# Performance work log

Hardware: AMD Instinct MI355X
Metric: run time of the kernel (lower is better)

## Reference

```python
import jax, jax.numpy as jnp
import numpy as np

NEG = -1e6  # masked_softmax fill value from the original code


def setup_inputs() -> dict:
    key = jax.random.key(0)
    ks = jax.random.split(key, 8)
    B, Q, K, Dq, Dk, Dv, H = 8, 256, 1024, 256, 256, 128, 128
    queries = jax.random.normal(ks[0], (B, Q, Dq), dtype=jnp.float32)
    keys = jax.random.normal(ks[1], (B, K, Dk), dtype=jnp.float32)
    values = jax.random.normal(ks[2], (B, K, Dv), dtype=jnp.float32)
    valid_lens = jax.random.randint(ks[3], (B,), 1, K + 1, dtype=jnp.int32)
    # learned params (Dense, use_bias=False): y = x @ W
    W_q = jax.random.normal(ks[4], (Dq, H), dtype=jnp.float32) / np.sqrt(Dq)
    W_k = jax.random.normal(ks[5], (Dk, H), dtype=jnp.float32) / np.sqrt(Dk)
    w_v = jax.random.normal(ks[6], (H,), dtype=jnp.float32) / np.sqrt(H)
    return {"queries": queries, "keys": keys, "values": values,
            "valid_lens": valid_lens, "W_q": W_q, "W_k": W_k, "w_v": w_v}


def reference(queries, keys, values, valid_lens, W_q, W_k, w_v):
    q = jnp.einsum('bqd,dh->bqh', queries, W_q)          # [B,Q,H]
    k = jnp.einsum('bkd,dh->bkh', keys, W_k)             # [B,K,H]
    features = jnp.tanh(q[:, :, None, :] + k[:, None, :, :])  # [B,Q,K,H]
    scores = jnp.einsum('bqkh,h->bqk', features, w_v)    # [B,Q,K]
    # masked softmax over last axis: positions >= valid_len set to -1e6
    K_len = scores.shape[-1]
    mask = jnp.arange(K_len)[None, None, :] < valid_lens[:, None, None]
    scores = jnp.where(mask, scores, NEG)
    attn = jax.nn.softmax(scores, axis=-1)
    return jnp.einsum('bqk,bkv->bqv', attn, values)      # [B,Q,Dv]
```

## Files before the change

kernel.cpp:

```cpp
#include <hip/hip_runtime.h>
#include <hip/hip_bf16.h>

#if defined(__has_builtin)
#if __has_builtin(__builtin_amdgcn_exp2f)
#define EXP2F __builtin_amdgcn_exp2f
#endif
#if __has_builtin(__builtin_amdgcn_rcpf)
#define RCPF __builtin_amdgcn_rcpf
#endif
#endif
#ifndef EXP2F
#define EXP2F exp2f
#endif
#ifndef RCPF
#define RCPF(x) (1.0f / (x))
#endif

#define B_  8
#define Q_  256
#define K_  1024
#define D_  256
#define H_  128
#define DV_ 128

#define CSL 2.8853900817779268f
#define L2E 1.4426950408889634f

#define QE_OFF   0
#define KE_OFF   262144
#define WPK_OFF  1310720
#define PART_OFF 1311744
#define PSZ      1310720

__global__ __launch_bounds__(256) void proj_split(
    const float* __restrict__ queries, const float* __restrict__ keys,
    const float* __restrict__ Wq, const float* __restrict__ Wk,
    float* __restrict__ part, int nchunk)
{
    __shared__ __align__(16) float As[64][68];
    __shared__ __align__(16) float Ws[64][128];

    const int tid = threadIdx.x;
    const int rt = blockIdx.x;
    const bool isQ = rt < 32;
    const int row0 = isQ ? rt * 64 : (rt - 32) * 64;
    const int crow0 = isQ ? row0 : row0 + 2048;
    const float* A = isQ ? (queries + row0 * D_) : (keys + row0 * D_);
    const float* W = isQ ? Wq : Wk;

    float acc[8][4];
#pragma unroll
    for (int i = 0; i < 8; i++)
#pragma unroll
        for (int j = 0; j < 4; j++) acc[i][j] = 0.f;

    const int rgrp = tid >> 5;
    const int c0 = (tid & 31) * 4;
    const int lr = tid & 63;
    const int ld = (tid >> 6) * 16;

    for (int ch = 0; ch < nchunk; ch++) {
        const int d0 = (blockIdx.y * nchunk + ch) * 64;
#pragma unroll
        for (int j = 0; j < 4; j++) {
            const float4 a = *(const float4*)&A[lr * D_ + d0 + ld + j * 4];
            As[ld + j * 4 + 0][lr] = a.x;
            As[ld + j * 4 + 1][lr] = a.y;
            As[ld + j * 4 + 2][lr] = a.z;
            As[ld + j * 4 + 3][lr] = a.w;
        }
#pragma unroll
        for (int l = 0; l < 8; l++) {
            const int idx = tid + l * 256;
            const int rr = idx >> 5, cc = (idx & 31) * 4;
            *(float4*)&Ws[rr][cc] = *(const float4*)&W[(d0 + rr) * H_ + cc];
        }
        __syncthreads();
#pragma unroll 4
        for (int d = 0; d < 64; d++) {
            const float4 w = *(const float4*)&Ws[d][c0];
            const float4 a0 = *(const float4*)&As[d][rgrp * 8];
            const float4 a1 = *(const float4*)&As[d][rgrp * 8 + 4];
            const float ar[8] = {a0.x, a0.y, a0.z, a0.w, a1.x, a1.y, a1.z, a1.w};
#pragma unroll
            for (int i = 0; i < 8; i++) {
                acc[i][0] = fmaf(ar[i], w.x, acc[i][0]);
                acc[i][1] = fmaf(ar[i], w.y, acc[i][1]);
                acc[i][2] = fmaf(ar[i], w.z, acc[i][2]);
                acc[i][3] = fmaf(ar[i], w.w, acc[i][3]);
            }
        }
        __syncthreads();
    }
    float* dst = part + (size_t)blockIdx.y * PSZ + (size_t)(crow0 + rgrp * 8) * H_ + c0;
#pragma unroll
    for (int i = 0; i < 8; i++)
        *(float4*)&dst[i * H_] = make_float4(acc[i][0], acc[i][1], acc[i][2], acc[i][3]);
}

__global__ __launch_bounds__(256) void finish_kernel(
    const float* __restrict__ part, int S,
    const float* __restrict__ w_v,
    float* __restrict__ qE, float* __restrict__ kET, float* __restrict__ wpk)
{
    __shared__ float T[128][33];
    const int tid = threadIdx.x;
    const int row0 = blockIdx.x * 32;
    const bool isQ = row0 < 2048;

    float e[16];
#pragma unroll
    for (int i = 0; i < 16; i++) {
        const int idx = row0 * H_ + tid + i * 256;
        float v = part[idx];
        for (int s = 1; s < S; s++) v += part[(size_t)s * PSZ + idx];
        e[i] = EXP2F(CSL * v);
    }
    if (isQ) {
#pragma unroll
        for (int i = 0; i < 16; i++) qE[row0 * H_ + tid + i * 256] = e[i];
    } else {
#pragma unroll
        for (int i = 0; i < 16; i++) {
            const int idx = tid + i * 256;
            T[idx & 127][idx >> 7] = e[i];
        }
        __syncthreads();
        const int krow0 = row0 - 2048;
        const int b = krow0 >> 10, k0 = krow0 & 1023;
        const int h = tid >> 1, kh = (tid & 1) * 16;
        float* dst = kET + (size_t)b * (H_ * K_) + (size_t)h * K_ + k0 + kh;
#pragma unroll
        for (int j = 0; j < 4; j++)
            *(float4*)&dst[j * 4] = make_float4(T[h][kh + j * 4], T[h][kh + j * 4 + 1],
                                                T[h][kh + j * 4 + 2], T[h][kh + j * 4 + 3]);
    }
    if (blockIdx.x == 0 && tid < 64) {
        const float w1 = -2.0f * L2E * w_v[2 * tid];
        const float w2 = -2.0f * L2E * w_v[2 * tid + 1];
        *(float4*)&wpk[tid * 4] = make_float4(w1, w2, w1 + w2, 0.f);
    }
}

__global__ void wpk_kernel(const float* __restrict__ w_v, float* __restrict__ wpk) {
    const int t = threadIdx.x;
    const float w1 = -2.0f * L2E * w_v[2 * t];
    const float w2 = -2.0f * L2E * w_v[2 * t + 1];
    *(float4*)&wpk[t * 4] = make_float4(w1, w2, w1 + w2, 0.f);
}

__global__ __launch_bounds__(256) void proj_direct(
    const float* __restrict__ queries, const float* __restrict__ keys,
    const float* __restrict__ Wq, const float* __restrict__ Wk,
    float* __restrict__ qE, float* __restrict__ kE)
{
    __shared__ __align__(16) float As[16][36];
    __shared__ __align__(16) float Ws[32][128];

    const int tid = threadIdx.x;
    const int blk = blockIdx.x;
    const bool isQ = blk < 128;
    const int row0 = isQ ? blk * 16 : (blk - 128) * 16;
    const float* A = isQ ? (queries + row0 * D_) : (keys + row0 * D_);
    const float* W = isQ ? Wq : Wk;

    float acc[8];
#pragma unroll
    for (int j = 0; j < 8; j++) acc[j] = 0.f;
    const int r = tid >> 4;
    const int c8 = (tid & 15) * 8;

    for (int d0 = 0; d0 < D_; d0 += 32) {
        if (tid < 128) {
            const int rr = tid >> 3, cc = (tid & 7) * 4;
            *(float4*)&As[rr][cc] = *(const float4*)&A[rr * D_ + d0 + cc];
        }
#pragma unroll
        for (int l = 0; l < 4; l++) {
            const int idx = tid + l * 256;
            const int rr = idx >> 5, cc = (idx & 31) * 4;
            *(float4*)&Ws[rr][cc] = *(const float4*)&W[(d0 + rr) * H_ + cc];
        }
        __syncthreads();
#pragma unroll
        for (int d = 0; d < 32; d++) {
            const float a = As[r][d];
            const float4 w0 = *(const float4*)&Ws[d][c8];
            const float4 w1 = *(const float4*)&Ws[d][c8 + 4];
            acc[0] = fmaf(a, w0.x, acc[0]); acc[1] = fmaf(a, w0.y, acc[1]);
            acc[2] = fmaf(a, w0.z, acc[2]); acc[3] = fmaf(a, w0.w, acc[3]);
            acc[4] = fmaf(a, w1.x, acc[4]); acc[5] = fmaf(a, w1.y, acc[5]);
            acc[6] = fmaf(a, w1.z, acc[6]); acc[7] = fmaf(a, w1.w, acc[7]);
        }
        __syncthreads();
    }
    float e[8];
#pragma unroll
    for (int j = 0; j < 8; j++) e[j] = EXP2F(CSL * acc[j]);
    if (isQ) {
        float* dst = qE + (row0 + r) * H_ + c8;
        *(float4*)dst = make_float4(e[0], e[1], e[2], e[3]);
        *(float4*)(dst + 4) = make_float4(e[4], e[5], e[6], e[7]);
    } else {
        const int krow = row0 + r;
        const int b = krow >> 10, k = krow & 1023;
        float* dst = kE + b * (H_ * K_) + c8 * K_ + k;
#pragma unroll
        for (int j = 0; j < 8; j++) dst[j * K_] = e[j];
    }
}

__global__ __launch_bounds__(1024, 8) void attn_kernel(
    const float* __restrict__ qE,
    const float* __restrict__ kET,
    const float* __restrict__ values,
    const int*   __restrict__ valid_lens,
    const float* __restrict__ wpk,
    float* __restrict__ out)
{
    __shared__ __align__(16) float sc[K_][4];
    __shared__ __align__(16) float red[16][4][128];
    __shared__ __align__(16) float psum[16][4];
    __shared__ float rl[4];

    const int tid = threadIdx.x;
    const int b  = blockIdx.y;
    const int q0 = blockIdx.x * 4;

    const float* q0p = qE + (b * Q_ + q0) * H_;
    const float* q1p = q0p + H_;
    const float* q2p = q0p + 2 * H_;
    const float* q3p = q0p + 3 * H_;
    const float* kb = kET + (size_t)b * (H_ * K_) + tid;

    float2 acc01 = make_float2(0.f, 0.f);
    float2 acc23 = make_float2(0.f, 0.f);

#pragma unroll 4
    for (int p = 0; p < 64; p++) {
        const float ek1 = kb[(2 * p) * K_];
        const float ek2 = kb[(2 * p + 1) * K_];
        const float4 wp = *(const float4*)&wpk[p * 4];
        const float2 qa = *(const float2*)&q0p[2 * p];
        const float2 qb = *(const float2*)&q1p[2 * p];
        const float2 qc = *(const float2*)&q2p[2 * p];
        const float2 qd = *(const float2*)&q3p[2 * p];
        {
            float2 x1 = make_float2(qa.x * ek1, qb.x * ek1);
            float2 x2 = make_float2(qa.y * ek2, qb.y * ek2);
            float2 e1 = make_float2(x1.x + 1.f, x1.y + 1.f);
            float2 d  = make_float2(fmaf(e1.x, x2.x, e1.x), fmaf(e1.y, x2.y, e1.y));
            float2 n  = make_float2(fmaf(wp.y, x1.x, wp.z), fmaf(wp.y, x1.y, wp.z));
            n = make_float2(fmaf(wp.x, x2.x, n.x), fmaf(wp.x, x2.y, n.y));
            acc01.x = fmaf(n.x, RCPF(d.x), acc01.x);
            acc01.y = fmaf(n.y, RCPF(d.y), acc01.y);
        }
        {
            float2 x1 = make_float2(qc.x * ek1, qd.x * ek1);
            float2 x2 = make_float2(qc.y * ek2, qd.y * ek2);
            float2 e1 = make_float2(x1.x + 1.f, x1.y + 1.f);
            float2 d  = make_float2(fmaf(e1.x, x2.x, e1.x), fmaf(e1.y, x2.y, e1.y));
            float2 n  = make_float2(fmaf(wp.y, x1.x, wp.z), fmaf(wp.y, x1.y, wp.z));
            n = make_float2(fmaf(wp.x, x2.x, n.x), fmaf(wp.x, x2.y, n.y));
            acc23.x = fmaf(n.x, RCPF(d.x), acc23.x);
            acc23.y = fmaf(n.y, RCPF(d.y), acc23.y);
        }
    }

    const int vl = valid_lens[b];
    const bool valid = tid < vl;
    float4 pv;
    pv.x = valid ? EXP2F(acc01.x) : 0.f;
    pv.y = valid ? EXP2F(acc01.y) : 0.f;
    pv.z = valid ? EXP2F(acc23.x) : 0.f;
    pv.w = valid ? EXP2F(acc23.y) : 0.f;
    *(float4*)&sc[tid][0] = pv;

    float4 s = pv;
#pragma unroll
    for (int sh = 32; sh > 0; sh >>= 1) {
        s.x += __shfl_xor(s.x, sh);
        s.y += __shfl_xor(s.y, sh);
        s.z += __shfl_xor(s.z, sh);
        s.w += __shfl_xor(s.w, sh);
    }
    const int lane = tid & 63, w = tid >> 6;
    if (lane == 0) *(float4*)&psum[w][0] = s;
    __syncthreads();
    if (tid < 4) {
        float t = 0.f;
#pragma unroll
        for (int ww = 0; ww < 16; ww++) t += psum[ww][tid];
        rl[tid] = RCPF(t);
    }

    const int vg = (tid & 31) * 4;
    const int kh = (tid >> 5) & 1;
    const int kc = tid >> 6;
    const float* vb = values + (size_t)b * (K_ * DV_) + vg;
    float av[4][4];
#pragma unroll
    for (int q = 0; q < 4; q++)
#pragma unroll
        for (int j = 0; j < 4; j++) av[q][j] = 0.f;
#pragma unroll 2
    for (int i = 0; i < 32; i++) {
        const int k = kc * 64 + i * 2 + kh;
        const float4 vv = *(const float4*)&vb[k * DV_];
        const float4 p = *(const float4*)&sc[k][0];
        av[0][0] = fmaf(p.x, vv.x, av[0][0]); av[0][1] = fmaf(p.x, vv.y, av[0][1]);
        av[0][2] = fmaf(p.x, vv.z, av[0][2]); av[0][3] = fmaf(p.x, vv.w, av[0][3]);
        av[1][0] = fmaf(p.y, vv.x, av[1][0]); av[1][1] = fmaf(p.y, vv.y, av[1][1]);
        av[1][2] = fmaf(p.y, vv.z, av[1][2]); av[1][3] = fmaf(p.y, vv.w, av[1][3]);
        av[2][0] = fmaf(p.z, vv.x, av[2][0]); av[2][1] = fmaf(p.z, vv.y, av[2][1]);
        av[2][2] = fmaf(p.z, vv.z, av[2][2]); av[2][3] = fmaf(p.z, vv.w, av[2][3]);
        av[3][0] = fmaf(p.w, vv.x, av[3][0]); av[3][1] = fmaf(p.w, vv.y, av[3][1]);
        av[3][2] = fmaf(p.w, vv.z, av[3][2]); av[3][3] = fmaf(p.w, vv.w, av[3][3]);
    }
#pragma unroll
    for (int q = 0; q < 4; q++)
#pragma unroll
        for (int j = 0; j < 4; j++) av[q][j] += __shfl_xor(av[q][j], 32);
    if (kh == 0) {
#pragma unroll
        for (int q = 0; q < 4; q++)
            *(float4*)&red[kc][q][vg] = make_float4(av[q][0], av[q][1], av[q][2], av[q][3]);
    }
    __syncthreads();

    if (tid < 512) {
        const int q = tid >> 7, v = tid & 127;
        float t = 0.f;
#pragma unroll
        for (int g = 0; g < 16; g++) t += red[g][q][v];
        out[(b * Q_ + q0 + q) * DV_ + v] = t * rl[q];
    }
}

extern "C" void kernel_launch(void* const* d_in, const int* in_sizes, int n_in,
                              void* d_out, int out_size, void* d_ws, size_t ws_size,
                              hipStream_t stream) {
    const float* queries    = (const float*)d_in[0];
    const float* keys       = (const float*)d_in[1];
    const float* values     = (const float*)d_in[2];
    const int*   valid_lens = (const int*)d_in[3];
    const float* W_q        = (const float*)d_in[4];
    const float* W_k        = (const float*)d_in[5];
    const float* w_v        = (const float*)d_in[6];
    float* out = (float*)d_out;

    float* ws  = (float*)d_ws;
    float* qE  = ws + QE_OFF;
    float* kET = ws + KE_OFF;
    float* wpk = ws + WPK_OFF;
    float* part = ws + PART_OFF;

    int S = 0;
    if (ws_size >= (size_t)(PART_OFF + 4 * (size_t)PSZ) * 4) S = 4;
    else if (ws_size >= (size_t)(PART_OFF + 2 * (size_t)PSZ) * 4) S = 2;
    else if (ws_size >= (size_t)(PART_OFF + 1 * (size_t)PSZ) * 4) S = 1;

    if (S > 0) {
        proj_split<<<dim3(160, S), 256, 0, stream>>>(queries, keys, W_q, W_k, part, 4 / S);
        finish_kernel<<<320, 256, 0, stream>>>(part, S, w_v, qE, kET, wpk);
    } else {
        proj_direct<<<640, 256, 0, stream>>>(queries, keys, W_q, W_k, qE, kET);
        wpk_kernel<<<1, 64, 0, stream>>>(w_v, wpk);
    }
    attn_kernel<<<dim3(Q_ / 4, B_), 1024, 0, stream>>>(qE, kET, values, valid_lens, wpk, out);
}
```

Before: 140.1 us.

## Fuse projection into one kernel, pack keys as float2, skip masked keys

Replaces the split-K projection and its separate finish kernel with a single projection kernel. That kernel applies the exponent and writes qE plus an h-pair-interleaved float2 key layout directly, which removes one launch and the partial-sum round trip. The attention kernel reads both key features of a pair with one float2 load, skips the score computation for keys beyond valid_len, and limits the P·V loop to valid keys. The single-kernel projection uses only 160 blocks with the full D reduction each, so it has less parallelism than the split version. Skipping work depends on the data-dependent valid lengths and causes divergence at the boundary.

```diff
diff --git a/kernel.cpp b/kernel.cpp
--- a/kernel.cpp
+++ b/kernel.cpp
@@ -29,45 +29,42 @@
 #define QE_OFF   0
 #define KE_OFF   262144
 #define WPK_OFF  1310720
-#define PART_OFF 1311744
-#define PSZ      1310720
-
-__global__ __launch_bounds__(256) void proj_split(
+
+__global__ __launch_bounds__(256) void proj_kernel(
     const float* __restrict__ queries, const float* __restrict__ keys,
     const float* __restrict__ Wq, const float* __restrict__ Wk,
-    float* __restrict__ part, int nchunk)
+    const float* __restrict__ w_v,
+    float* __restrict__ qE, float2* __restrict__ kET2, float* __restrict__ wpk)
 {
     __shared__ __align__(16) float As[64][68];
     __shared__ __align__(16) float Ws[64][128];
 
     const int tid = threadIdx.x;
-    const int rt = blockIdx.x;
-    const bool isQ = rt < 32;
-    const int row0 = isQ ? rt * 64 : (rt - 32) * 64;
-    const int crow0 = isQ ? row0 : row0 + 2048;
+    const int blk = blockIdx.x;
+    const bool isQ = blk < 32;
+    const int row0 = isQ ? blk * 64 : (blk - 32) * 64;
     const float* A = isQ ? (queries + row0 * D_) : (keys + row0 * D_);
     const float* W = isQ ? Wq : Wk;
 
-    float acc[8][4];
-#pragma unroll
-    for (int i = 0; i < 8; i++)
-#pragma unroll
-        for (int j = 0; j < 4; j++) acc[i][j] = 0.f;
-
-    const int rgrp = tid >> 5;
-    const int c0 = (tid & 31) * 4;
-    const int lr = tid & 63;
-    const int ld = (tid >> 6) * 16;
-
-    for (int ch = 0; ch < nchunk; ch++) {
-        const int d0 = (blockIdx.y * nchunk + ch) * 64;
+    float acc[4][8];
+#pragma unroll
+    for (int i = 0; i < 4; i++)
+#pragma unroll
+        for (int j = 0; j < 8; j++) acc[i][j] = 0.f;
+
+    const int lr  = tid & 63;
+    const int ldb = (tid >> 6) * 16;
+    const int r4  = (tid >> 4) * 4;
+    const int c8  = (tid & 15) * 8;
+
+    for (int d0 = 0; d0 < D_; d0 += 64) {
 #pragma unroll
         for (int j = 0; j < 4; j++) {
-            const float4 a = *(const float4*)&A[lr * D_ + d0 + ld + j * 4];
-            As[ld + j * 4 + 0][lr] = a.x;
-            As[ld + j * 4 + 1][lr] = a.y;
-            As[ld + j * 4 + 2][lr] = a.z;
-            As[ld + j * 4 + 3][lr] = a.w;
+            const float4 a = *(const float4*)&A[lr * D_ + d0 + ldb + j * 4];
+            As[ldb + j * 4 + 0][lr] = a.x;
+            As[ldb + j * 4 + 1][lr] = a.y;
+            As[ldb + j * 4 + 2][lr] = a.z;
+            As[ldb + j * 4 + 3][lr] = a.w;
         }
 #pragma unroll
         for (int l = 0; l < 8; l++) {
@@ -78,141 +75,54 @@
         __syncthreads();
 #pragma unroll 4
         for (int d = 0; d < 64; d++) {
-            const float4 w = *(const float4*)&Ws[d][c0];
-            const float4 a0 = *(const float4*)&As[d][rgrp * 8];
-            const float4 a1 = *(const float4*)&As[d][rgrp * 8 + 4];
-            const float ar[8] = {a0.x, a0.y, a0.z, a0.w, a1.x, a1.y, a1.z, a1.w};
-#pragma unroll
-            for (int i = 0; i < 8; i++) {
-                acc[i][0] = fmaf(ar[i], w.x, acc[i][0]);
-                acc[i][1] = fmaf(ar[i], w.y, acc[i][1]);
-                acc[i][2] = fmaf(ar[i], w.z, acc[i][2]);
-                acc[i][3] = fmaf(ar[i], w.w, acc[i][3]);
+            const float4 a4 = *(const float4*)&As[d][r4];
+            const float4 w0 = *(const float4*)&Ws[d][c8];
+            const float4 w1 = *(const float4*)&Ws[d][c8 + 4];
+            const float ar[4] = {a4.x, a4.y, a4.z, a4.w};
+#pragma unroll
+            for (int i = 0; i < 4; i++) {
+                acc[i][0] = fmaf(ar[i], w0.x, acc[i][0]);
+                acc[i][1] = fmaf(ar[i], w0.y, acc[i][1]);
+                acc[i][2] = fmaf(ar[i], w0.z, acc[i][2]);
+                acc[i][3] = fmaf(ar[i], w0.w, acc[i][3]);
+                acc[i][4] = fmaf(ar[i], w1.x, acc[i][4]);
+                acc[i][5] = fmaf(ar[i], w1.y, acc[i][5]);
+                acc[i][6] = fmaf(ar[i], w1.z, acc[i][6]);
+                acc[i][7] = fmaf(ar[i], w1.w, acc[i][7]);
             }
         }
         __syncthreads();
     }
-    float* dst = part + (size_t)blockIdx.y * PSZ + (size_t)(crow0 + rgrp * 8) * H_ + c0;
-#pragma unroll
-    for (int i = 0; i < 8; i++)
-        *(float4*)&dst[i * H_] = make_float4(acc[i][0], acc[i][1], acc[i][2], acc[i][3]);
-}
-
-__global__ __launch_bounds__(256) void finish_kernel(
-    const float* __restrict__ part, int S,
-    const float* __restrict__ w_v,
-    float* __restrict__ qE, float* __restrict__ kET, float* __restrict__ wpk)
-{
-    __shared__ float T[128][33];
-    const int tid = threadIdx.x;
-    const int row0 = blockIdx.x * 32;
-    const bool isQ = row0 < 2048;
-
-    float e[16];
-#pragma unroll
-    for (int i = 0; i < 16; i++) {
-        const int idx = row0 * H_ + tid + i * 256;
-        float v = part[idx];
-        for (int s = 1; s < S; s++) v += part[(size_t)s * PSZ + idx];
-        e[i] = EXP2F(CSL * v);
-    }
-    if (isQ) {
-#pragma unroll
-        for (int i = 0; i < 16; i++) qE[row0 * H_ + tid + i * 256] = e[i];
-    } else {
-#pragma unroll
-        for (int i = 0; i < 16; i++) {
-            const int idx = tid + i * 256;
-            T[idx & 127][idx >> 7] = e[i];
-        }
-        __syncthreads();
-        const int krow0 = row0 - 2048;
-        const int b = krow0 >> 10, k0 = krow0 & 1023;
-        const int h = tid >> 1, kh = (tid & 1) * 16;
-        float* dst = kET + (size_t)b * (H_ * K_) + (size_t)h * K_ + k0 + kh;
-#pragma unroll
-        for (int j = 0; j < 4; j++)
-            *(float4*)&dst[j * 4] = make_float4(T[h][kh + j * 4], T[h][kh + j * 4 + 1],
-                                                T[h][kh + j * 4 + 2], T[h][kh + j * 4 + 3]);
-    }
-    if (blockIdx.x == 0 && tid < 64) {
+
+#pragma unroll
+    for (int i = 0; i < 4; i++) {
+        float e[8];
+#pragma unroll
+        for (int j = 0; j < 8; j++) e[j] = EXP2F(CSL * acc[i][j]);
+        const int row = row0 + r4 + i;
+        if (isQ) {
+            float* dst = qE + row * H_ + c8;
+            *(float4*)dst = make_float4(e[0], e[1], e[2], e[3]);
+            *(float4*)(dst + 4) = make_float4(e[4], e[5], e[6], e[7]);
+        } else {
+            const int b = row >> 10, k = row & 1023;
+            float2* dst = kET2 + (size_t)(b * 64 + (c8 >> 1)) * K_ + k;
+#pragma unroll
+            for (int jj = 0; jj < 4; jj++)
+                dst[jj * K_] = make_float2(e[2 * jj], e[2 * jj + 1]);
+        }
+    }
+
+    if (blk == 0 && tid < 64) {
         const float w1 = -2.0f * L2E * w_v[2 * tid];
         const float w2 = -2.0f * L2E * w_v[2 * tid + 1];
         *(float4*)&wpk[tid * 4] = make_float4(w1, w2, w1 + w2, 0.f);
     }
 }
 
-__global__ void wpk_kernel(const float* __restrict__ w_v, float* __restrict__ wpk) {
-    const int t = threadIdx.x;
-    const float w1 = -2.0f * L2E * w_v[2 * t];
-    const float w2 = -2.0f * L2E * w_v[2 * t + 1];
-    *(float4*)&wpk[t * 4] = make_float4(w1, w2, w1 + w2, 0.f);
-}
-
-__global__ __launch_bounds__(256) void proj_direct(
-    const float* __restrict__ queries, const float* __restrict__ keys,
-    const float* __restrict__ Wq, const float* __restrict__ Wk,
-    float* __restrict__ qE, float* __restrict__ kE)
-{
-    __shared__ __align__(16) float As[16][36];
-    __shared__ __align__(16) float Ws[32][128];
-
-    const int tid = threadIdx.x;
-    const int blk = blockIdx.x;
-    const bool isQ = blk < 128;
-    const int row0 = isQ ? blk * 16 : (blk - 128) * 16;
-    const float* A = isQ ? (queries + row0 * D_) : (keys + row0 * D_);
-    const float* W = isQ ? Wq : Wk;
-
-    float acc[8];
-#pragma unroll
-    for (int j = 0; j < 8; j++) acc[j] = 0.f;
-    const int r = tid >> 4;
-    const int c8 = (tid & 15) * 8;
-
-    for (int d0 = 0; d0 < D_; d0 += 32) {
-        if (tid < 128) {
-            const int rr = tid >> 3, cc = (tid & 7) * 4;
-            *(float4*)&As[rr][cc] = *(const float4*)&A[rr * D_ + d0 + cc];
-        }
-#pragma unroll
-        for (int l = 0; l < 4; l++) {
-            const int idx = tid + l * 256;
-            const int rr = idx >> 5, cc = (idx & 31) * 4;
-            *(float4*)&Ws[rr][cc] = *(const float4*)&W[(d0 + rr) * H_ + cc];
-        }
-        __syncthreads();
-#pragma unroll
-        for (int d = 0; d < 32; d++) {
-            const float a = As[r][d];
-            const float4 w0 = *(const float4*)&Ws[d][c8];
-            const float4 w1 = *(const float4*)&Ws[d][c8 + 4];
-            acc[0] = fmaf(a, w0.x, acc[0]); acc[1] = fmaf(a, w0.y, acc[1]);
-            acc[2] = fmaf(a, w0.z, acc[2]); acc[3] = fmaf(a, w0.w, acc[3]);
-            acc[4] = fmaf(a, w1.x, acc[4]); acc[5] = fmaf(a, w1.y, acc[5]);
-            acc[6] = fmaf(a, w1.z, acc[6]); acc[7] = fmaf(a, w1.w, acc[7]);
-        }
-        __syncthreads();
-    }
-    float e[8];
-#pragma unroll
-    for (int j = 0; j < 8; j++) e[j] = EXP2F(CSL * acc[j]);
-    if (isQ) {
-        float* dst = qE + (row0 + r) * H_ + c8;
-        *(float4*)dst = make_float4(e[0], e[1], e[2], e[3]);
-        *(float4*)(dst + 4) = make_float4(e[4], e[5], e[6], e[7]);
-    } else {
-        const int krow = row0 + r;
-        const int b = krow >> 10, k = krow & 1023;
-        float* dst = kE + b * (H_ * K_) + c8 * K_ + k;
-#pragma unroll
-        for (int j = 0; j < 8; j++) dst[j * K_] = e[j];
-    }
-}
-
 __global__ __launch_bounds__(1024, 8) void attn_kernel(
     const float* __restrict__ qE,
-    const float* __restrict__ kET,
+    const float2* __restrict__ kET2,
     const float* __restrict__ values,
     const int*   __restrict__ valid_lens,
     const float* __restrict__ wpk,
@@ -226,48 +136,49 @@
     const int tid = threadIdx.x;
     const int b  = blockIdx.y;
     const int q0 = blockIdx.x * 4;
+    const int vl = valid_lens[b];
 
     const float* q0p = qE + (b * Q_ + q0) * H_;
     const float* q1p = q0p + H_;
     const float* q2p = q0p + 2 * H_;
     const float* q3p = q0p + 3 * H_;
-    const float* kb = kET + (size_t)b * (H_ * K_) + tid;
+    const float2* kb2 = kET2 + (size_t)(b * 64) * K_ + tid;
 
     float2 acc01 = make_float2(0.f, 0.f);
     float2 acc23 = make_float2(0.f, 0.f);
 
+    if (tid < vl) {
 #pragma unroll 4
-    for (int p = 0; p < 64; p++) {
-        const float ek1 = kb[(2 * p) * K_];
-        const float ek2 = kb[(2 * p + 1) * K_];
-        const float4 wp = *(const float4*)&wpk[p * 4];
-        const float2 qa = *(const float2*)&q0p[2 * p];
-        const float2 qb = *(const float2*)&q1p[2 * p];
-        const float2 qc = *(const float2*)&q2p[2 * p];
-        const float2 qd = *(const float2*)&q3p[2 * p];
-        {
-            float2 x1 = make_float2(qa.x * ek1, qb.x * ek1);
-            float2 x2 = make_float2(qa.y * ek2, qb.y * ek2);
-            float2 e1 = make_float2(x1.x + 1.f, x1.y + 1.f);
-            float2 d  = make_float2(fmaf(e1.x, x2.x, e1.x), fmaf(e1.y, x2.y, e1.y));
-            float2 n  = make_float2(fmaf(wp.y, x1.x, wp.z), fmaf(wp.y, x1.y, wp.z));
-            n = make_float2(fmaf(wp.x, x2.x, n.x), fmaf(wp.x, x2.y, n.y));
-            acc01.x = fmaf(n.x, RCPF(d.x), acc01.x);
-            acc01.y = fmaf(n.y, RCPF(d.y), acc01.y);
-        }
-        {
-            float2 x1 = make_float2(qc.x * ek1, qd.x * ek1);
-            float2 x2 = make_float2(qc.y * ek2, qd.y * ek2);
-            float2 e1 = make_float2(x1.x + 1.f, x1.y + 1.f);
-            float2 d  = make_float2(fmaf(e1.x, x2.x, e1.x), fmaf(e1.y, x2.y, e1.y));
-            float2 n  = make_float2(fmaf(wp.y, x1.x, wp.z), fmaf(wp.y, x1.y, wp.z));
-            n = make_float2(fmaf(wp.x, x2.x, n.x), fmaf(wp.x, x2.y, n.y));
-            acc23.x = fmaf(n.x, RCPF(d.x), acc23.x);
-            acc23.y = fmaf(n.y, RCPF(d.y), acc23.y);
-        }
-    }
-
-    const int vl = valid_lens[b];
+        for (int p = 0; p < 64; p++) {
+            const float2 ek = kb2[(size_t)p * K_];
+            const float4 wp = *(const float4*)&wpk[p * 4];
+            const float2 qa = *(const float2*)&q0p[2 * p];
+            const float2 qb = *(const float2*)&q1p[2 * p];
+            const float2 qc = *(const float2*)&q2p[2 * p];
+            const float2 qd = *(const float2*)&q3p[2 * p];
+            {
+                float2 x1 = make_float2(qa.x * ek.x, qb.x * ek.x);
+                float2 x2 = make_float2(qa.y * ek.y, qb.y * ek.y);
+                float2 e1 = make_float2(x1.x + 1.f, x1.y + 1.f);
+                float2 d  = make_float2(fmaf(e1.x, x2.x, e1.x), fmaf(e1.y, x2.y, e1.y));
+                float2 n  = make_float2(fmaf(wp.y, x1.x, wp.z), fmaf(wp.y, x1.y, wp.z));
+                n = make_float2(fmaf(wp.x, x2.x, n.x), fmaf(wp.x, x2.y, n.y));
+                acc01.x = fmaf(n.x, RCPF(d.x), acc01.x);
+                acc01.y = fmaf(n.y, RCPF(d.y), acc01.y);
+            }
+            {
+                float2 x1 = make_float2(qc.x * ek.x, qd.x * ek.x);
+                float2 x2 = make_float2(qc.y * ek.y, qd.y * ek.y);
+                float2 e1 = make_float2(x1.x + 1.f, x1.y + 1.f);
+                float2 d  = make_float2(fmaf(e1.x, x2.x, e1.x), fmaf(e1.y, x2.y, e1.y));
+                float2 n  = make_float2(fmaf(wp.y, x1.x, wp.z), fmaf(wp.y, x1.y, wp.z));
+                n = make_float2(fmaf(wp.x, x2.x, n.x), fmaf(wp.x, x2.y, n.y));
+                acc23.x = fmaf(n.x, RCPF(d.x), acc23.x);
+                acc23.y = fmaf(n.y, RCPF(d.y), acc23.y);
+            }
+        }
+    }
+
     const bool valid = tid < vl;
     float4 pv;
     pv.x = valid ? EXP2F(acc01.x) : 0.f;
@@ -303,8 +214,11 @@
     for (int q = 0; q < 4; q++)
 #pragma unroll
         for (int j = 0; j < 4; j++) av[q][j] = 0.f;
+
+    const int rem = vl - kc * 64 - kh;
+    const int imax = rem <= 0 ? 0 : (((rem + 1) >> 1) > 32 ? 32 : ((rem + 1) >> 1));
 #pragma unroll 2
-    for (int i = 0; i < 32; i++) {
+    for (int i = 0; i < imax; i++) {
         const int k = kc * 64 + i * 2 + kh;
         const float4 vv = *(const float4*)&vb[k * DV_];
         const float4 p = *(const float4*)&sc[k][0];
@@ -349,23 +263,11 @@
     const float* w_v        = (const float*)d_in[6];
     float* out = (float*)d_out;
 
-    float* ws  = (float*)d_ws;
-    float* qE  = ws + QE_OFF;
-    float* kET = ws + KE_OFF;
-    float* wpk = ws + WPK_OFF;
-    float* part = ws + PART_OFF;
-
-    int S = 0;
-    if (ws_size >= (size_t)(PART_OFF + 4 * (size_t)PSZ) * 4) S = 4;
-    else if (ws_size >= (size_t)(PART_OFF + 2 * (size_t)PSZ) * 4) S = 2;
-    else if (ws_size >= (size_t)(PART_OFF + 1 * (size_t)PSZ) * 4) S = 1;
-
-    if (S > 0) {
-        proj_split<<<dim3(160, S), 256, 0, stream>>>(queries, keys, W_q, W_k, part, 4 / S);
-        finish_kernel<<<320, 256, 0, stream>>>(part, S, w_v, qE, kET, wpk);
-    } else {
-        proj_direct<<<640, 256, 0, stream>>>(queries, keys, W_q, W_k, qE, kET);
-        wpk_kernel<<<1, 64, 0, stream>>>(w_v, wpk);
-    }
-    attn_kernel<<<dim3(Q_ / 4, B_), 1024, 0, stream>>>(qE, kET, values, valid_lens, wpk, out);
+    float*  ws   = (float*)d_ws;
+    float*  qE   = ws + QE_OFF;
+    float2* kET2 = (float2*)(ws + KE_OFF);
+    float*  wpk  = ws + WPK_OFF;
+
+    proj_kernel<<<160, 256, 0, stream>>>(queries, keys, W_q, W_k, w_v, qE, kET2, wpk);
+    attn_kernel<<<dim3(Q_ / 4, B_), 1024, 0, stream>>>(qE, kET2, values, valid_lens, wpk, out);
 }
```

Measured after the change: 121.4 us. -13.4%, faster.
